# Kernel tuning notes

Hardware: AMD Instinct MI355X
Metric: run time of the kernel (lower is better)

Reference implementation:

```python
import jax, jax.numpy as jnp
import numpy as np
from jax import lax

EPS = 1e-5

def binarize(x):
    # sign() forward, straight-through (identity) backward, like BinarizeConv2d's .data trick
    return x + lax.stop_gradient(jnp.sign(x) - x)

def conv_nchw(x, w, stride, pad):
    return lax.conv_general_dilated(
        x, w, window_strides=(stride, stride), padding=((pad, pad), (pad, pad)),
        dimension_numbers=('NCHW', 'OIHW', 'NCHW'))

def batchnorm_train(x, gamma, beta):
    # training-mode BN: per-channel batch mean / biased variance over (N,H,W)
    mean = jnp.mean(x, axis=(0, 2, 3), keepdims=True)
    var = jnp.mean((x - mean) ** 2, axis=(0, 2, 3), keepdims=True)
    xhat = (x - mean) * lax.rsqrt(var + EPS)
    return xhat * gamma[None, :, None, None] + beta[None, :, None, None]

def hardtanh(x):
    return jnp.clip(x, -1.0, 1.0)

def setup_inputs() -> dict:
    key = jax.random.key(0)
    ks = jax.random.split(key, 7)
    N, Cin, Cout, H, W = 32, 64, 64, 128, 128
    x = jax.random.normal(ks[0], (N, Cin, H, W), dtype=jnp.float32)
    w1 = jax.random.normal(ks[1], (Cout, Cin, 3, 3), dtype=jnp.float32) * 0.05
    w2 = jax.random.normal(ks[2], (Cout, Cout, 3, 3), dtype=jnp.float32) * 0.05
    g1 = jnp.ones((Cout,), dtype=jnp.float32)
    b1 = jnp.zeros((Cout,), dtype=jnp.float32)
    g2 = jnp.ones((Cout,), dtype=jnp.float32)
    b2 = jnp.zeros((Cout,), dtype=jnp.float32)
    return {"x": x, "w1": w1, "g1": g1, "b1": b1, "w2": w2, "g2": g2, "b2": b2}

def reference(x, w1, g1, b1, w2, g2, b2):
    # conv1: binarized input (C=64 != 3) and binarized weights
    out = conv_nchw(binarize(x), binarize(w1), stride=1, pad=1)
    out = hardtanh(batchnorm_train(out, g1, b1))
    # conv2: 3x3, stride 1 (stride==1 branch)
    out = conv_nchw(binarize(out), binarize(w2), stride=1, pad=1)
    out = batchnorm_train(out, g2, b2)
    # identity shortcut (stride==1 and in_planes==planes)
    out = out + x
    return hardtanh(out)
```

## Files before the change

### kernel.cpp

```cpp
#include <hip/hip_runtime.h>
#include <stdint.h>

typedef unsigned long long u64;
typedef unsigned int u32;

#define Nn 32
#define Cc 64
#define Hh 128
#define Ww 128
#define HPAD 130
#define WPAD 130
#define NHW_TOT (Nn*Hh*Ww)
#define NBIN 16

__device__ __forceinline__ float2 compute_ab(const u64* __restrict__ sum, const u64* __restrict__ sq,
        const float* __restrict__ g, const float* __restrict__ bet, int c) {
    long long Sv = 0, Qv = 0;
    #pragma unroll
    for (int b = 0; b < NBIN; ++b) {
        Sv += (long long)sum[b * 64 + c];
        Qv += (long long)sq[b * 64 + c];
    }
    double mean = (double)Sv / (double)NHW_TOT;
    double var = (double)Qv / (double)NHW_TOT - mean * mean;
    double invstd = 1.0 / sqrt(var + 1e-5);
    double a = (double)g[c] * invstd;
    double b_ = (double)bet[c] - a * mean;
    return make_float2((float)a, (float)b_);
}

#define BORDER_PER_IMG 516
#define BORDER_TOT (Nn * BORDER_PER_IMG)
#define PREP_EXTRA (1152 + 2 * BORDER_TOT + 4 * NBIN * 64)

__global__ __launch_bounds__(256) void prep_kernel(const float* __restrict__ x,
        const float* __restrict__ w1, const float* __restrict__ w2,
        u64* __restrict__ xpad, u64* __restrict__ ypad,
        u64* __restrict__ w1b, u64* __restrict__ w2b, u64* __restrict__ stats) {
    if (blockIdx.x < 512) {
        int t = blockIdx.x * 256 + threadIdx.x;
        int P = t * 4;
        int row = P >> 7, w0 = P & 127;
        int n = row >> 7, h = row & 127;
        const float4* xp4 = (const float4*)(x + ((size_t)n * Cc * Hh + h) * Ww + w0);
        u32 lo0 = 0, lo1 = 0, lo2 = 0, lo3 = 0, hi0 = 0, hi1 = 0, hi2 = 0, hi3 = 0;
        #pragma unroll 8
        for (int c = 0; c < 32; ++c) {
            float4 v = xp4[c * (Hh * Ww / 4)];
            lo0 |= (__float_as_uint(v.x) >> 31) << c;
            lo1 |= (__float_as_uint(v.y) >> 31) << c;
            lo2 |= (__float_as_uint(v.z) >> 31) << c;
            lo3 |= (__float_as_uint(v.w) >> 31) << c;
        }
        #pragma unroll 8
        for (int c = 32; c < 64; ++c) {
            float4 v = xp4[c * (Hh * Ww / 4)];
            hi0 |= (__float_as_uint(v.x) >> 31) << (c - 32);
            hi1 |= (__float_as_uint(v.y) >> 31) << (c - 32);
            hi2 |= (__float_as_uint(v.z) >> 31) << (c - 32);
            hi3 |= (__float_as_uint(v.w) >> 31) << (c - 32);
        }
        u64* dst = xpad + ((size_t)n * HPAD + h + 1) * WPAD + w0 + 1;
        dst[0] = ((u64)hi0 << 32) | lo0;
        dst[1] = ((u64)hi1 << 32) | lo1;
        dst[2] = ((u64)hi2 << 32) | lo2;
        dst[3] = ((u64)hi3 << 32) | lo3;
    } else {
        int t = (blockIdx.x - 512) * 256 + threadIdx.x;
        int stride = (gridDim.x - 512) * 256;
        for (int i = t; i < PREP_EXTRA; i += stride) {
            if (i < 1152) {
                int set = i / 576, idx = i - set * 576;
                const float* src = set ? w2 : w1;
                u64* db = set ? w2b : w1b;
                int co = idx / 9, tap = idx - co * 9;
                const float* p = src + (size_t)co * 576 + tap;
                u32 lo = 0, hi = 0;
                #pragma unroll
                for (int ci = 0; ci < 32; ++ci)
                    lo |= (__float_as_uint(p[ci * 9]) >> 31) << ci;
                #pragma unroll
                for (int ci = 32; ci < 64; ++ci)
                    hi |= (__float_as_uint(p[ci * 9]) >> 31) << (ci - 32);
                db[idx] = ((u64)hi << 32) | lo;
            } else if (i < 1152 + 2 * BORDER_TOT) {
                int z = i - 1152;
                u64* buf = (z < BORDER_TOT) ? xpad : ypad;
                int k = (z < BORDER_TOT) ? z : z - BORDER_TOT;
                int img = k / BORDER_PER_IMG, j = k - img * BORDER_PER_IMG;
                size_t base = (size_t)img * HPAD * WPAD;
                size_t off;
                if (j < 130)      off = j;
                else if (j < 260) off = (size_t)(HPAD - 1) * WPAD + (j - 130);
                else {
                    int k2 = j - 260;
                    off = (size_t)(1 + (k2 >> 1)) * WPAD + ((k2 & 1) ? (WPAD - 1) : 0);
                }
                buf[base + off] = 0ull;
            } else {
                stats[i - 1152 - 2 * BORDER_TOT] = 0ull;
            }
        }
    }
}

__device__ __forceinline__ void conv4(const u64* __restrict__ L0, const u64* __restrict__ L1,
                                      const u64* __restrict__ L2, int w,
                                      const u64 W[9], int corrMid, int v[4]) {
    u64 a[6], b[6], c[6];
    #pragma unroll
    for (int j = 0; j < 3; ++j) {
        ulonglong2 pa = *(const ulonglong2*)&L0[w + 2 * j];
        ulonglong2 pb = *(const ulonglong2*)&L1[w + 2 * j];
        ulonglong2 pc = *(const ulonglong2*)&L2[w + 2 * j];
        a[2 * j] = pa.x; a[2 * j + 1] = pa.y;
        b[2 * j] = pb.x; b[2 * j + 1] = pb.y;
        c[2 * j] = pc.x; c[2 * j + 1] = pc.y;
    }
    #pragma unroll
    for (int px = 0; px < 4; ++px) {
        int p0 = __popcll(a[px] ^ W[0]) + __popcll(a[px + 1] ^ W[1]) + __popcll(a[px + 2] ^ W[2]);
        int p1 = __popcll(b[px] ^ W[3]) + __popcll(b[px + 1] ^ W[4]) + __popcll(b[px + 2] ^ W[5]);
        int p2 = __popcll(c[px] ^ W[6]) + __popcll(c[px + 1] ^ W[7]) + __popcll(c[px + 2] ^ W[8]);
        v[px] = 576 - 2 * (p0 + p1 + p2) - corrMid;
    }
}

struct LaneCtx {
    u64 W[9];
    int corrMid, corrW0, corrW127;
};

__device__ __forceinline__ void lane_setup(LaneCtx& C, const u64* __restrict__ wb,
                                           int lane, int h) {
    #pragma unroll
    for (int t = 0; t < 9; ++t) C.W[t] = wb[lane * 9 + t];
    int wc[9];
    #pragma unroll
    for (int t = 0; t < 9; ++t) wc[t] = 64 - 2 * __popcll(C.W[t]);
    int tT = wc[0] + wc[1] + wc[2], tB = wc[6] + wc[7] + wc[8];
    int tL = wc[0] + wc[3] + wc[6], tR = wc[2] + wc[5] + wc[8];
    bool fT = (h == 0), fB = (h == 127);
    C.corrMid  = (fT ? tT : 0) + (fB ? tB : 0);
    C.corrW0   = tL - (fT ? wc[0] : 0) - (fB ? wc[6] : 0);
    C.corrW127 = tR - (fT ? wc[2] : 0) - (fB ? wc[8] : 0);
}

__device__ __forceinline__ void load_win(u64* __restrict__ win, const u64* __restrict__ inpad,
                                         int n, int hp, int half, int tid) {
    const u64* src = inpad + ((size_t)n * HPAD + hp * 2) * WPAD + half * 64;
    for (int i = tid; i < 264; i += 128) {
        int r = i / 66, c = i - r * 66;
        win[r * 68 + c] = src[(size_t)r * WPAD + c];
    }
}

template<bool SPILL>
__global__ __launch_bounds__(128) void conv_statsT(const u64* __restrict__ inpad,
        const u64* __restrict__ wb, u64* __restrict__ gsum, u64* __restrict__ gsq,
        short* __restrict__ v16) {
    __shared__ u64 win[4 * 68];
    __shared__ int r32[256];
    int tid = threadIdx.x;
    int lane = tid & 63;
    int wv = __builtin_amdgcn_readfirstlane(tid >> 6);
    int blk = blockIdx.x;
    int half = blk & 1;
    int hp = (blk >> 1) & 63;
    int n = blk >> 7;
    int h = hp * 2 + wv;
    load_win(win, inpad, n, hp, half, tid);
    LaneCtx C;
    lane_setup(C, wb, lane, h);
    __syncthreads();
    const u64* L0 = &win[wv * 68];
    const u64* L1 = L0 + 68;
    const u64* L2 = L0 + 136;
    short* vrow = SPILL ? (v16 + (((size_t)(n * Hh + h) * Ww) + half * 64) * 64 + lane) : nullptr;
    int s = 0, q = 0;
    for (int w = 0; w < 64; w += 4) {
        int v[4];
        conv4(L0, L1, L2, w, C.W, C.corrMid, v);
        if (half == 0 && w == 0)  v[0] -= C.corrW0;
        if (half == 1 && w == 60) v[3] -= C.corrW127;
        #pragma unroll
        for (int px = 0; px < 4; ++px) {
            s += v[px];
            q += __mul24(v[px], v[px]);
            if (SPILL) vrow[(size_t)(w + px) * 64] = (short)v[px];
        }
    }
    __syncthreads();
    r32[wv * 64 + lane] = s;
    r32[128 + wv * 64 + lane] = q;
    __syncthreads();
    if (wv == 0) {
        int S = r32[lane] + r32[64 + lane];
        int Q = r32[128 + lane] + r32[192 + lane];
        int bin = blk & (NBIN - 1);
        atomicAdd(&gsum[bin * 64 + lane], (u64)(long long)S);
        atomicAdd(&gsq[bin * 64 + lane], (u64)(long long)Q);
    }
}

__global__ __launch_bounds__(256) void signpack_v(const short* __restrict__ v16,
        const u64* __restrict__ sum, const u64* __restrict__ sq,
        const float* __restrict__ g, const float* __restrict__ bet,
        u64* __restrict__ ypad) {
    int tid = threadIdx.x;
    int lane = tid & 63;
    int wv = tid >> 6;
    int grow = blockIdx.x * 2 + (wv >> 1);
    int base = (wv & 1) * 64;
    int n = grow >> 7, h = grow & 127;
    float2 ab = compute_ab(sum, sq, g, bet, lane);
    const short* vr = v16 + ((size_t)grow * Ww + base) * 64;
    u64* drow = ypad + ((size_t)n * HPAD + h + 1) * WPAD + 1;
    u64 myw = 0;
    #pragma unroll 8
    for (int px = 0; px < 64; ++px) {
        float tv = fmaf((float)vr[(size_t)px * 64 + lane], ab.x, ab.y);
        u64 bal = __ballot(tv < 0.0f);
        if (lane == px) myw = bal;
    }
    drow[base + lane] = myw;
}

__global__ __launch_bounds__(128) void signpack_h(const u64* __restrict__ inpad,
        const u64* __restrict__ wb, const u64* __restrict__ sum, const u64* __restrict__ sq,
        const float* __restrict__ g, const float* __restrict__ bet,
        u64* __restrict__ ypad) {
    __shared__ u64 win[4 * 68];
    int tid = threadIdx.x;
    int lane = tid & 63;
    int wv = __builtin_amdgcn_readfirstlane(tid >> 6);
    int blk = blockIdx.x;
    int half = blk & 1;
    int hp = (blk >> 1) & 63;
    int n = blk >> 7;
    int h = hp * 2 + wv;
    load_win(win, inpad, n, hp, half, tid);
    LaneCtx C;
    lane_setup(C, wb, lane, h);
    float2 ab = compute_ab(sum, sq, g, bet, lane);
    __syncthreads();
    const u64* L0 = &win[wv * 68];
    const u64* L1 = L0 + 68;
    const u64* L2 = L0 + 136;
    u64 myw = 0;
    for (int w = 0; w < 64; w += 4) {
        int v[4];
        conv4(L0, L1, L2, w, C.W, C.corrMid, v);
        if (half == 0 && w == 0)  v[0] -= C.corrW0;
        if (half == 1 && w == 60) v[3] -= C.corrW127;
        #pragma unroll
        for (int px = 0; px < 4; ++px) {
            float t = fmaf((float)v[px], ab.x, ab.y);
            u64 bal = __ballot(t < 0.0f);
            if (lane == w + px) myw = bal;
        }
    }
    ypad[((size_t)n * HPAD + h + 1) * WPAD + 1 + half * 64 + lane] = myw;
}

__global__ __launch_bounds__(128) void final5_kernel(const u64* __restrict__ inpad,
        const u64* __restrict__ wb, const u64* __restrict__ sum, const u64* __restrict__ sq,
        const float* __restrict__ g, const float* __restrict__ bet,
        const float* __restrict__ x, float* __restrict__ out) {
    __shared__ u64 win[4 * 68];
    __shared__ short T[2][64 * 36];
    __shared__ float2 absh[64];
    int tid = threadIdx.x;
    int lane = tid & 63;
    int wv = __builtin_amdgcn_readfirstlane(tid >> 6);
    int blk = blockIdx.x;
    int half = blk & 1;
    int hp = (blk >> 1) & 63;
    int n = blk >> 7;
    int h = hp * 2 + wv;
    load_win(win, inpad, n, hp, half, tid);
    LaneCtx C;
    lane_setup(C, wb, lane, h);
    if (tid < 64) absh[tid] = compute_ab(sum, sq, g, bet, tid);
    __syncthreads();
    const u64* L0 = &win[wv * 68];
    const u64* L1 = L0 + 68;
    const u64* L2 = L0 + 136;
    short* Tw = T[wv];
    int p4 = lane & 7;
    int cosub = lane >> 3;
    size_t base_nch = ((size_t)n * Cc * Hh + h) * Ww;
    for (int w = 0; w < 64; w += 4) {
        int v[4];
        conv4(L0, L1, L2, w, C.W, C.corrMid, v);
        if (half == 0 && w == 0)  v[0] -= C.corrW0;
        if (half == 1 && w == 60) v[3] -= C.corrW127;
        short4 sv;
        sv.x = (short)v[0]; sv.y = (short)v[1]; sv.z = (short)v[2]; sv.w = (short)v[3];
        *(short4*)&Tw[lane * 36 + (w & 31)] = sv;
        if ((w & 31) == 28) {
            int w0g = half * 64 + (w & ~31);
            #pragma unroll 8
            for (int st = 0; st < 8; ++st) {
                int co = st * 8 + cosub;
                short4 tv = *(const short4*)&Tw[co * 36 + p4 * 4];
                float2 cab = absh[co];
                size_t idx = base_nch + (size_t)co * (Hh * Ww) + w0g + p4 * 4;
                float4 xv = *(const float4*)(x + idx);
                float4 yv;
                yv.x = fminf(1.0f, fmaxf(-1.0f, fmaf((float)tv.x, cab.x, cab.y) + xv.x));
                yv.y = fminf(1.0f, fmaxf(-1.0f, fmaf((float)tv.y, cab.x, cab.y) + xv.y));
                yv.z = fminf(1.0f, fmaxf(-1.0f, fmaf((float)tv.z, cab.x, cab.y) + xv.z));
                yv.w = fminf(1.0f, fmaxf(-1.0f, fmaf((float)tv.w, cab.x, cab.y) + xv.w));
                *(float4*)(out + idx) = yv;
            }
        }
    }
}

extern "C" void kernel_launch(void* const* d_in, const int* in_sizes, int n_in,
                              void* d_out, int out_size, void* d_ws, size_t ws_size,
                              hipStream_t stream) {
    const float* x  = (const float*)d_in[0];
    const float* w1 = (const float*)d_in[1];
    const float* g1 = (const float*)d_in[2];
    const float* b1 = (const float*)d_in[3];
    const float* w2 = (const float*)d_in[4];
    const float* g2 = (const float*)d_in[5];
    const float* b2 = (const float*)d_in[6];
    float* out = (float*)d_out;
    char* ws = (char*)d_ws;

    constexpr size_t SZ_PAD   = (size_t)Nn * HPAD * WPAD * sizeof(u64);
    constexpr size_t OFF_YPAD = SZ_PAD;
    constexpr size_t OFF_STAT = 2 * SZ_PAD;
    constexpr size_t SZ_STAT  = (size_t)NBIN * 64 * 8;
    constexpr size_t OFF_W1B  = OFF_STAT + 4 * SZ_STAT;
    constexpr size_t OFF_W2B  = OFF_W1B + 576 * 8;
    constexpr size_t OFF_V16  = OFF_W2B + 576 * 8;
    constexpr size_t SZ_V16   = (size_t)Nn * Hh * Ww * 64 * 2;
    constexpr size_t WS_SMALL = OFF_V16;
    constexpr size_t WS_FULL  = OFF_V16 + SZ_V16;

    if (ws_size < WS_SMALL) return;
    bool spill = (ws_size >= WS_FULL);

    u64* xpad = (u64*)(ws);
    u64* ypad = (u64*)(ws + OFF_YPAD);
    u64* stats = (u64*)(ws + OFF_STAT);
    u64* gsum1 = (u64*)(ws + OFF_STAT);
    u64* gsq1  = (u64*)(ws + OFF_STAT + SZ_STAT);
    u64* gsum2 = (u64*)(ws + OFF_STAT + 2 * SZ_STAT);
    u64* gsq2  = (u64*)(ws + OFF_STAT + 3 * SZ_STAT);
    u64* w1b  = (u64*)(ws + OFF_W1B);
    u64* w2b  = (u64*)(ws + OFF_W2B);
    short* v16 = (short*)(ws + OFF_V16);

    prep_kernel<<<530, 256, 0, stream>>>(x, w1, w2, xpad, ypad, w1b, w2b, stats);
    if (spill) {
        conv_statsT<true><<<4096, 128, 0, stream>>>(xpad, w1b, gsum1, gsq1, v16);
        signpack_v<<<2048, 256, 0, stream>>>(v16, gsum1, gsq1, g1, b1, ypad);
    } else {
        conv_statsT<false><<<4096, 128, 0, stream>>>(xpad, w1b, gsum1, gsq1, nullptr);
        signpack_h<<<4096, 128, 0, stream>>>(xpad, w1b, gsum1, gsq1, g1, b1, ypad);
    }
    conv_statsT<false><<<4096, 128, 0, stream>>>(ypad, w2b, gsum2, gsq2, nullptr);
    final5_kernel<<<4096, 128, 0, stream>>>(ypad, w2b, gsum2, gsq2, g2, b2, x, out);
}
```

Baseline: 209.4 us.

## Process two full rows per 256-thread block to share the input window

The conv, signpack and final kernels now run 256-thread blocks that each cover two full output rows, both halves, instead of 128-thread blocks covering half-rows. The four-row binarized input window is loaded once per block, which removes the duplicated halo loads across half-width blocks and halves the block count and the number of stats atomics. The final kernel's transpose tile shrinks from 32 to 16 pixels so output stores happen more often in smaller chunks. In exchange, per-block shared memory grows and there are fewer, larger blocks.

```diff
diff --git a/kernel.cpp b/kernel.cpp
--- a/kernel.cpp
+++ b/kernel.cpp
@@ -146,36 +146,37 @@
     C.corrW127 = tR - (fT ? wc[2] : 0) - (fB ? wc[8] : 0);
 }
 
-__device__ __forceinline__ void load_win(u64* __restrict__ win, const u64* __restrict__ inpad,
-                                         int n, int hp, int half, int tid) {
-    const u64* src = inpad + ((size_t)n * HPAD + hp * 2) * WPAD + half * 64;
-    for (int i = tid; i < 264; i += 128) {
-        int r = i / 66, c = i - r * 66;
-        win[r * 68 + c] = src[(size_t)r * WPAD + c];
+__device__ __forceinline__ void load_win4(u64* __restrict__ win, const u64* __restrict__ inpad,
+                                          int n, int rp, int tid) {
+    const u64* src = inpad + ((size_t)n * HPAD + rp * 2) * WPAD;
+    for (int i = tid; i < 520; i += 256) {
+        int r = i / 130, c = i - r * 130;
+        win[r * 132 + c] = src[(size_t)r * WPAD + c];
     }
 }
 
 template<bool SPILL>
-__global__ __launch_bounds__(128) void conv_statsT(const u64* __restrict__ inpad,
+__global__ __launch_bounds__(256) void conv_stats4(const u64* __restrict__ inpad,
         const u64* __restrict__ wb, u64* __restrict__ gsum, u64* __restrict__ gsq,
         short* __restrict__ v16) {
-    __shared__ u64 win[4 * 68];
-    __shared__ int r32[256];
+    __shared__ u64 win[4 * 132];
+    __shared__ int r32[512];
     int tid = threadIdx.x;
     int lane = tid & 63;
     int wv = __builtin_amdgcn_readfirstlane(tid >> 6);
     int blk = blockIdx.x;
-    int half = blk & 1;
-    int hp = (blk >> 1) & 63;
-    int n = blk >> 7;
-    int h = hp * 2 + wv;
-    load_win(win, inpad, n, hp, half, tid);
+    int rp = blk & 63;
+    int n = blk >> 6;
+    int half = wv & 1;
+    int r = wv >> 1;
+    int h = rp * 2 + r;
+    load_win4(win, inpad, n, rp, tid);
     LaneCtx C;
     lane_setup(C, wb, lane, h);
     __syncthreads();
-    const u64* L0 = &win[wv * 68];
-    const u64* L1 = L0 + 68;
-    const u64* L2 = L0 + 136;
+    const u64* L0 = &win[r * 132 + half * 64];
+    const u64* L1 = L0 + 132;
+    const u64* L2 = L0 + 264;
     short* vrow = SPILL ? (v16 + (((size_t)(n * Hh + h) * Ww) + half * 64) * 64 + lane) : nullptr;
     int s = 0, q = 0;
     for (int w = 0; w < 64; w += 4) {
@@ -192,11 +193,11 @@
     }
     __syncthreads();
     r32[wv * 64 + lane] = s;
-    r32[128 + wv * 64 + lane] = q;
+    r32[256 + wv * 64 + lane] = q;
     __syncthreads();
     if (wv == 0) {
-        int S = r32[lane] + r32[64 + lane];
-        int Q = r32[128 + lane] + r32[192 + lane];
+        int S = r32[lane] + r32[64 + lane] + r32[128 + lane] + r32[192 + lane];
+        int Q = r32[256 + lane] + r32[320 + lane] + r32[384 + lane] + r32[448 + lane];
         int bin = blk & (NBIN - 1);
         atomicAdd(&gsum[bin * 64 + lane], (u64)(long long)S);
         atomicAdd(&gsq[bin * 64 + lane], (u64)(long long)Q);
@@ -226,27 +227,28 @@
     drow[base + lane] = myw;
 }
 
-__global__ __launch_bounds__(128) void signpack_h(const u64* __restrict__ inpad,
+__global__ __launch_bounds__(256) void signpack_h(const u64* __restrict__ inpad,
         const u64* __restrict__ wb, const u64* __restrict__ sum, const u64* __restrict__ sq,
         const float* __restrict__ g, const float* __restrict__ bet,
         u64* __restrict__ ypad) {
-    __shared__ u64 win[4 * 68];
+    __shared__ u64 win[4 * 132];
     int tid = threadIdx.x;
     int lane = tid & 63;
     int wv = __builtin_amdgcn_readfirstlane(tid >> 6);
     int blk = blockIdx.x;
-    int half = blk & 1;
-    int hp = (blk >> 1) & 63;
-    int n = blk >> 7;
-    int h = hp * 2 + wv;
-    load_win(win, inpad, n, hp, half, tid);
+    int rp = blk & 63;
+    int n = blk >> 6;
+    int half = wv & 1;
+    int r = wv >> 1;
+    int h = rp * 2 + r;
+    load_win4(win, inpad, n, rp, tid);
     LaneCtx C;
     lane_setup(C, wb, lane, h);
     float2 ab = compute_ab(sum, sq, g, bet, lane);
     __syncthreads();
-    const u64* L0 = &win[wv * 68];
-    const u64* L1 = L0 + 68;
-    const u64* L2 = L0 + 136;
+    const u64* L0 = &win[r * 132 + half * 64];
+    const u64* L1 = L0 + 132;
+    const u64* L2 = L0 + 264;
     u64 myw = 0;
     for (int w = 0; w < 64; w += 4) {
         int v[4];
@@ -263,32 +265,33 @@
     ypad[((size_t)n * HPAD + h + 1) * WPAD + 1 + half * 64 + lane] = myw;
 }
 
-__global__ __launch_bounds__(128) void final5_kernel(const u64* __restrict__ inpad,
+__global__ __launch_bounds__(256) void final7_kernel(const u64* __restrict__ inpad,
         const u64* __restrict__ wb, const u64* __restrict__ sum, const u64* __restrict__ sq,
         const float* __restrict__ g, const float* __restrict__ bet,
         const float* __restrict__ x, float* __restrict__ out) {
-    __shared__ u64 win[4 * 68];
-    __shared__ short T[2][64 * 36];
+    __shared__ u64 win[4 * 132];
+    __shared__ short T[4][64 * 20];
     __shared__ float2 absh[64];
     int tid = threadIdx.x;
     int lane = tid & 63;
     int wv = __builtin_amdgcn_readfirstlane(tid >> 6);
     int blk = blockIdx.x;
-    int half = blk & 1;
-    int hp = (blk >> 1) & 63;
-    int n = blk >> 7;
-    int h = hp * 2 + wv;
-    load_win(win, inpad, n, hp, half, tid);
+    int rp = blk & 63;
+    int n = blk >> 6;
+    int half = wv & 1;
+    int r = wv >> 1;
+    int h = rp * 2 + r;
+    load_win4(win, inpad, n, rp, tid);
     LaneCtx C;
     lane_setup(C, wb, lane, h);
     if (tid < 64) absh[tid] = compute_ab(sum, sq, g, bet, tid);
     __syncthreads();
-    const u64* L0 = &win[wv * 68];
-    const u64* L1 = L0 + 68;
-    const u64* L2 = L0 + 136;
+    const u64* L0 = &win[r * 132 + half * 64];
+    const u64* L1 = L0 + 132;
+    const u64* L2 = L0 + 264;
     short* Tw = T[wv];
-    int p4 = lane & 7;
-    int cosub = lane >> 3;
+    int p4 = lane & 3;
+    int cosub = lane >> 2;
     size_t base_nch = ((size_t)n * Cc * Hh + h) * Ww;
     for (int w = 0; w < 64; w += 4) {
         int v[4];
@@ -297,13 +300,13 @@
         if (half == 1 && w == 60) v[3] -= C.corrW127;
         short4 sv;
         sv.x = (short)v[0]; sv.y = (short)v[1]; sv.z = (short)v[2]; sv.w = (short)v[3];
-        *(short4*)&Tw[lane * 36 + (w & 31)] = sv;
-        if ((w & 31) == 28) {
-            int w0g = half * 64 + (w & ~31);
-            #pragma unroll 8
-            for (int st = 0; st < 8; ++st) {
-                int co = st * 8 + cosub;
-                short4 tv = *(const short4*)&Tw[co * 36 + p4 * 4];
+        *(short4*)&Tw[lane * 20 + (w & 15)] = sv;
+        if ((w & 15) == 12) {
+            int w0g = half * 64 + (w & ~15);
+            #pragma unroll
+            for (int st = 0; st < 4; ++st) {
+                int co = st * 16 + cosub;
+                short4 tv = *(const short4*)&Tw[co * 20 + p4 * 4];
                 float2 cab = absh[co];
                 size_t idx = base_nch + (size_t)co * (Hh * Ww) + w0g + p4 * 4;
                 float4 xv = *(const float4*)(x + idx);
@@ -358,12 +361,12 @@
 
     prep_kernel<<<530, 256, 0, stream>>>(x, w1, w2, xpad, ypad, w1b, w2b, stats);
     if (spill) {
-        conv_statsT<true><<<4096, 128, 0, stream>>>(xpad, w1b, gsum1, gsq1, v16);
+        conv_stats4<true><<<2048, 256, 0, stream>>>(xpad, w1b, gsum1, gsq1, v16);
         signpack_v<<<2048, 256, 0, stream>>>(v16, gsum1, gsq1, g1, b1, ypad);
     } else {
-        conv_statsT<false><<<4096, 128, 0, stream>>>(xpad, w1b, gsum1, gsq1, nullptr);
-        signpack_h<<<4096, 128, 0, stream>>>(xpad, w1b, gsum1, gsq1, g1, b1, ypad);
-    }
-    conv_statsT<false><<<4096, 128, 0, stream>>>(ypad, w2b, gsum2, gsq2, nullptr);
-    final5_kernel<<<4096, 128, 0, stream>>>(ypad, w2b, gsum2, gsq2, g2, b2, x, out);
-}
+        conv_stats4<false><<<2048, 256, 0, stream>>>(xpad, w1b, gsum1, gsq1, nullptr);
+        signpack_h<<<2048, 256, 0, stream>>>(xpad, w1b, gsum1, gsq1, g1, b1, ypad);
+    }
+    conv_stats4<false><<<2048, 256, 0, stream>>>(ypad, w2b, gsum2, gsq2, nullptr);
+    final7_kernel<<<2048, 256, 0, stream>>>(ypad, w2b, gsum2, gsq2, g2, b2, x, out);
+}
```

Measured after the change: 233.8 us. 1.12x slower.
